# Kernel optimization log

Hardware: AMD Instinct MI355X
Metric: run time of the kernel (lower is better)

The kernel has to match this reference:

```python
import jax, jax.numpy as jnp
import numpy as np

GAMMAS = (0.01, 0.1, 1.0, 10.0, 100.0)
FOCAL_GAMMA = 2.0
SMOOTH = 0.1
TASK_W = (0.4, 0.3, 0.3)
A_RECON, A_ORTH, A_ADV = 1.0, 0.1, 0.1
NUM_DOMAINS = 4
NUM_LABELS1 = 4


def focal_smooth(logits, targets, maskf):
    # FocalLoss.forward with smoothing > 0, masked mean
    n_classes = logits.shape[1]
    log_p = jax.nn.log_softmax(logits, axis=1)
    p = jnp.exp(log_p)
    onehot = jax.nn.one_hot(targets, n_classes, dtype=logits.dtype)
    smooth = onehot * (1.0 - SMOOTH) + SMOOTH / n_classes
    ce = -(smooth * log_p).sum(axis=1)
    pt = jnp.take_along_axis(p, targets[:, None], axis=1)[:, 0]
    loss = ce * (1.0 - pt) ** FOCAL_GAMMA
    return (loss * maskf).sum() / jnp.maximum(maskf.sum(), 1.0)


def ce_masked(logits, targets, maskf):
    log_p = jax.nn.log_softmax(logits, axis=1)
    nll = -jnp.take_along_axis(log_p, targets[:, None], axis=1)[:, 0]
    return (nll * maskf).sum() / jnp.maximum(maskf.sum(), 1.0)


def cond_mmd(feats, domains, labels, maskf):
    # Global pairwise sq-distance matrix; multi-gamma RBF kernels summed.
    sq = (feats ** 2).sum(axis=-1)                      # (B,)
    Dmat = sq[:, None] + sq[None, :] - 2.0 * feats @ feats.T  # (B,B)
    Ksum = jnp.zeros_like(Dmat)
    for g in GAMMAS:
        Ksum = Ksum + jnp.exp(-g * Dmat)
    loss = jnp.asarray(0.0, feats.dtype)
    count = jnp.asarray(0.0, feats.dtype)
    for lab in range(NUM_LABELS1):
        lm = (labels == lab).astype(feats.dtype) * maskf
        for d1 in range(NUM_DOMAINS):
            m1 = lm * (domains == d1).astype(feats.dtype)
            n1 = m1.sum()
            Km1 = Ksum @ m1
            for d2 in range(d1 + 1, NUM_DOMAINS):
                m2 = lm * (domains == d2).astype(feats.dtype)
                n2 = m2.sum()
                valid = (n1 > 1) & (n2 > 1)
                term = (m1 @ Km1) / jnp.maximum(n1, 1.0) ** 2 \
                     + (m2 @ (Ksum @ m2)) / jnp.maximum(n2, 1.0) ** 2 \
                     - 2.0 * (m2 @ Km1) / jnp.maximum(n1 * n2, 1.0)
                loss = loss + jnp.where(valid, term, 0.0)
                count = count + valid.astype(feats.dtype)
    return loss / jnp.maximum(count, 1.0)


def hsic(c, s):
    n = c.shape[0]
    c = c / jnp.maximum(jnp.linalg.norm(c, axis=-1, keepdims=True), 1e-12)
    s = s / jnp.maximum(jnp.linalg.norm(s, axis=-1, keepdims=True), 1e-12)
    K = c @ c.T
    L = s @ s.T
    Kc = K - K.mean(axis=0, keepdims=True) - K.mean(axis=1, keepdims=True) + K.mean()
    Lc = L - L.mean(axis=0, keepdims=True) - L.mean(axis=1, keepdims=True) + L.mean()
    return (Kc * Lc).sum() / (n - 1) ** 2


def setup_inputs() -> dict:
    key = jax.random.key(0)
    ks = jax.random.split(key, 20)
    B, D, H = 4096, 256, 768
    inp = {
        'logits1': jax.random.normal(ks[0], (B, 4), jnp.float32),
        'labels1': jax.random.randint(ks[1], (B,), 0, 4),
        'logits2': jax.random.normal(ks[2], (B, 6), jnp.float32),
        'labels2': jax.random.randint(ks[3], (B,), 0, 6),
        'logits3': jax.random.normal(ks[4], (B, 3), jnp.float32),
        'labels3': jax.random.randint(ks[5], (B,), 0, 3),
        'c_v': jax.random.normal(ks[6], (B, D), jnp.float32),
        's_v': jax.random.normal(ks[7], (B, D), jnp.float32),
        'c_t': jax.random.normal(ks[8], (B, D), jnp.float32),
        's_t': jax.random.normal(ks[9], (B, D), jnp.float32),
        'v_sv': jax.random.normal(ks[10], (B, NUM_DOMAINS), jnp.float32),
        'v_st': jax.random.normal(ks[11], (B, NUM_DOMAINS), jnp.float32),
        'domain_labels': jax.random.randint(ks[12], (B,), 0, NUM_DOMAINS),
        'mask': jnp.ones((B,), dtype=bool),
        'h_img_recon': jax.random.normal(ks[13], (B, H), jnp.float32),
        'h_img_orig': jax.random.normal(ks[14], (B, H), jnp.float32),
        'h_txt_recon': jax.random.normal(ks[15], (B, H), jnp.float32),
        'h_txt_orig': jax.random.normal(ks[16], (B, H), jnp.float32),
    }
    return inp


def reference(logits1, labels1, logits2, labels2, logits3, labels3,
              c_v, s_v, c_t, s_t, v_sv, v_st, domain_labels, mask,
              h_img_recon, h_img_orig, h_txt_recon, h_txt_orig):
    maskf = mask.astype(jnp.float32)
    total = jnp.asarray(0.0, jnp.float32)
    # classification (focal + label smoothing), per-task weighted
    total = total + TASK_W[0] * focal_smooth(logits1, labels1, maskf)
    total = total + TASK_W[1] * focal_smooth(logits2, labels2, maskf)
    total = total + TASK_W[2] * focal_smooth(logits3, labels3, maskf)
    # adversarial: CE on spurious domain logits + conditional MMD on causal feats
    l_adv_s = ce_masked(v_sv, domain_labels, maskf) + ce_masked(v_st, domain_labels, maskf)
    l_adv_c = cond_mmd(c_v, domain_labels, labels1, maskf) \
            + cond_mmd(c_t, domain_labels, labels1, maskf)
    total = total + A_ADV * (l_adv_s + l_adv_c)
    # orthogonality (HSIC), on unmasked features as in source
    l_orth = hsic(c_v, s_v) + hsic(c_t, s_t)
    total = total + A_ORTH * l_orth
    # reconstruction MSE
    l_recon = jnp.mean((h_img_recon - h_img_orig) ** 2) + jnp.mean((h_txt_recon - h_txt_orig) ** 2)
    total = total + A_RECON * l_recon
    return total
```

## Files before the change

kernel.cpp:

```cpp
#include <hip/hip_runtime.h>
#include <hip/hip_bf16.h>


typedef short bf16x8 __attribute__((ext_vector_type(8)));
typedef float f32x4 __attribute__((ext_vector_type(4)));
typedef unsigned long long u64;
typedef unsigned int u32;

static constexpr int D = 256;
static constexpr int H = 768;
static constexpr int NG = 16;
static constexpr float FX32 = 4294967296.f;
static constexpr float IFX32 = 2.3283064365386963e-10f;

__device__ inline void gAddFx(u64* p, float v) {
  long long q = (long long)llroundf(v * FX32);
  atomicAdd(p, (u64)q);
}
__device__ inline float fxToF(u64 v) { return (float)(long long)v * IFX32; }

__device__ inline float focal_n(const float* x, int n, int tgt,
                                float s_over_n, float oms) {
  float mx = x[0];
  for (int c = 1; c < n; ++c) mx = fmaxf(mx, x[c]);
  float se = 0.f, sx = 0.f;
  for (int c = 0; c < n; ++c) { se += __expf(x[c] - mx); sx += x[c]; }
  float logZ = mx + __logf(se);
  float ce = logZ - oms * x[tgt] - s_over_n * sx;
  float pt = __expf(x[tgt] - logZ);
  float om = 1.f - pt;
  return ce * om * om;
}

extern "C" __global__ __launch_bounds__(256) void k_pre(
    const void* __restrict__ mask, const int* __restrict__ y1,
    const int* __restrict__ dom,
    const float* __restrict__ l1, const float* __restrict__ l2,
    const float* __restrict__ l3, const int* __restrict__ y2,
    const int* __restrict__ y3,
    const float* __restrict__ vsv, const float* __restrict__ vst,
    const float* __restrict__ cv, const float* __restrict__ sv,
    const float* __restrict__ ct, const float* __restrict__ st,
    const float* __restrict__ ir, const float* __restrict__ io,
    const float* __restrict__ trc, const float* __restrict__ to,
    u64* SA, u64* GCU, u64* U64,
    int* gid, float* sq, float* inv, unsigned short* bf, u32* CNTB,
    int B, int N4, int NA, int NB) {
  __shared__ u32 sh3[3];
  __shared__ u32 cnt[17];
  __shared__ int redi[4];
  __shared__ float redf[4];
  __shared__ float redf5[5][4];
  __shared__ float ub[4][64][4];
  int bid = blockIdx.x;
  int t = threadIdx.x;

  if (bid < NA) {
    if (t < 3) sh3[t] = 0;
    if (t < 17) cnt[t] = 0;
    __syncthreads();
    u32 a = 0, b2 = 0, cd = 0;
    if (t * 16 + 15 < B) {
      uint4 wv = ((const uint4*)mask)[t];
      u32 ws[4] = {wv.x, wv.y, wv.z, wv.w};
      #pragma unroll
      for (int j = 0; j < 4; ++j) {
        a |= ws[j] & 0xffu; b2 |= ws[j] & 0xff00u; cd |= ws[j] & 0xffff0000u;
      }
    }
    if (a) atomicOr(&sh3[0], 1u);
    if (b2) atomicOr(&sh3[1], 1u);
    if (cd) atomicOr(&sh3[2], 1u);
    __syncthreads();
    int mode;
    if ((sh3[1] | sh3[2]) == 0) mode = 0;
    else if (sh3[0] == 0 && sh3[1] == 0) mode = 1;
    else mode = 2;
    int r = bid * 256 + t;
    int mi = 0;
    float s[5] = {0.f, 0.f, 0.f, 0.f, 0.f};
    if (r < B) {
      if (mode == 0)      mi = ((const int*)mask)[r] ? 1 : 0;
      else if (mode == 1) mi = (((const float*)mask)[r] != 0.f) ? 1 : 0;
      else                mi = ((const unsigned char*)mask)[r] ? 1 : 0;
      int g = -1;
      if (mi) { g = y1[r] * 4 + dom[r]; atomicAdd(&cnt[g], 1u); }
      else atomicAdd(&cnt[16], 1u);
      gid[r] = g;
      if (mi) {
        float x[6];
        for (int c = 0; c < 4; ++c) x[c] = l1[r * 4 + c];
        s[0] = focal_n(x, 4, y1[r], 0.1f / 4.f, 0.9f);
        for (int c = 0; c < 6; ++c) x[c] = l2[r * 6 + c];
        s[1] = focal_n(x, 6, y2[r], 0.1f / 6.f, 0.9f);
        for (int c = 0; c < 3; ++c) x[c] = l3[r * 3 + c];
        s[2] = focal_n(x, 3, y3[r], 0.1f / 3.f, 0.9f);
        int d = dom[r];
        for (int c = 0; c < 4; ++c) x[c] = vsv[r * 4 + c];
        {
          float mx = fmaxf(fmaxf(x[0], x[1]), fmaxf(x[2], x[3]));
          float se = __expf(x[0]-mx)+__expf(x[1]-mx)+__expf(x[2]-mx)+__expf(x[3]-mx);
          s[3] = mx + __logf(se) - x[d];
        }
        for (int c = 0; c < 4; ++c) x[c] = vst[r * 4 + c];
        {
          float mx = fmaxf(fmaxf(x[0], x[1]), fmaxf(x[2], x[3]));
          float se = __expf(x[0]-mx)+__expf(x[1]-mx)+__expf(x[2]-mx)+__expf(x[3]-mx);
          s[4] = mx + __logf(se) - x[d];
        }
      }
    }
    int v = mi;
    #pragma unroll
    for (int o = 32; o > 0; o >>= 1) {
      v += __shfl_down(v, o);
      #pragma unroll
      for (int k = 0; k < 5; ++k) s[k] += __shfl_down(s[k], o);
    }
    if ((t & 63) == 0) {
      redi[t >> 6] = v;
      #pragma unroll
      for (int k = 0; k < 5; ++k) redf5[k][t >> 6] = s[k];
    }
    __syncthreads();
    if (t == 0) {
      atomicAdd(&SA[5], (u64)(redi[0] + redi[1] + redi[2] + redi[3]));
      #pragma unroll
      for (int k = 0; k < 5; ++k)
        gAddFx(&SA[k], redf5[k][0] + redf5[k][1] + redf5[k][2] + redf5[k][3]);
    }
    if (t < NG && cnt[t]) atomicAdd(&GCU[t], (u64)cnt[t]);
    if (t < 17) CNTB[bid * 17 + t] = cnt[t];
  } else if (bid < NA + NB) {
    int b = bid - NA;
    int perF = NB >> 2;
    int f = b / perF;
    int rb = b - f * perF;
    const float* p = (f == 0) ? cv : (f == 1) ? sv : (f == 2) ? ct : st;
    int w = t >> 6, L = t & 63;
    float up0 = 0.f, up1 = 0.f, up2 = 0.f, up3 = 0.f;
    for (int bt = 0; bt < 2; ++bt) {
      int rbase = rb * 32 + w * 8 + bt * 4;
      float4 vv[4];
      #pragma unroll
      for (int i = 0; i < 4; ++i)
        vv[i] = ((const float4*)(p + (size_t)(rbase + i) * D))[L];
      float ss[4];
      #pragma unroll
      for (int i = 0; i < 4; ++i)
        ss[i] = vv[i].x * vv[i].x + vv[i].y * vv[i].y
              + vv[i].z * vv[i].z + vv[i].w * vv[i].w;
      #pragma unroll
      for (int o = 32; o > 0; o >>= 1) {
        #pragma unroll
        for (int i = 0; i < 4; ++i) ss[i] += __shfl_down(ss[i], o);
      }
      #pragma unroll
      for (int i = 0; i < 4; ++i) ss[i] = __shfl(ss[i], 0);
      #pragma unroll
      for (int i = 0; i < 4; ++i) {
        int r = rbase + i;
        float iv = 1.f / fmaxf(sqrtf(ss[i]), 1e-12f);
        if ((f & 1) == 0) {
          int fi = f >> 1;
          alignas(8) __hip_bfloat16 hb[4];
          hb[0] = __float2bfloat16(vv[i].x); hb[1] = __float2bfloat16(vv[i].y);
          hb[2] = __float2bfloat16(vv[i].z); hb[3] = __float2bfloat16(vv[i].w);
          *(uint2*)(bf + ((size_t)fi * B + r) * D + L * 4) = *(uint2*)hb;
          if (L == 0) sq[fi * B + r] = ss[i];
        }
        if (L == 0) inv[f * B + r] = iv;
        up0 += vv[i].x * iv; up1 += vv[i].y * iv;
        up2 += vv[i].z * iv; up3 += vv[i].w * iv;
      }
    }
    ub[w][L][0] = up0; ub[w][L][1] = up1; ub[w][L][2] = up2; ub[w][L][3] = up3;
    __syncthreads();
    if (t < 64) {
      u64* Uf = U64 + f * D + 4 * t;
      #pragma unroll
      for (int j = 0; j < 4; ++j) {
        float s4 = ub[0][t][j] + ub[1][t][j] + ub[2][t][j] + ub[3][t][j];
        gAddFx(Uf + j, s4);
      }
    }
  } else {
    int cidx = bid - (NA + NB);
    int j = cidx >> 9;
    int cb = cidx & 511;
    const float4* A  = (const float4*)(j ? trc : ir);
    const float4* Bp = (const float4*)(j ? to : io);
    int CH = (N4 + 511) >> 9;
    int base = cb * CH;
    int end = min(base + CH, N4);
    float acc = 0.f;
    int idx = base + t;
    for (; idx + 256 < end; idx += 512) {
      float4 a0 = A[idx],       b0 = Bp[idx];
      float4 a1 = A[idx + 256], b1 = Bp[idx + 256];
      float dx0 = a0.x-b0.x, dy0 = a0.y-b0.y, dz0 = a0.z-b0.z, dw0 = a0.w-b0.w;
      float dx1 = a1.x-b1.x, dy1 = a1.y-b1.y, dz1 = a1.z-b1.z, dw1 = a1.w-b1.w;
      acc += dx0*dx0 + dy0*dy0 + dz0*dz0 + dw0*dw0
           + dx1*dx1 + dy1*dy1 + dz1*dz1 + dw1*dw1;
    }
    if (idx < end) {
      float4 a = A[idx], b = Bp[idx];
      float dx = a.x-b.x, dy = a.y-b.y, dz = a.z-b.z, dw = a.w-b.w;
      acc += dx*dx + dy*dy + dz*dz + dw*dw;
    }
    #pragma unroll
    for (int o = 32; o > 0; o >>= 1) acc += __shfl_down(acc, o);
    if ((t & 63) == 0) redf[t >> 6] = acc;
    __syncthreads();
    if (t == 0) gAddFx(&SA[6 + j], redf[0] + redf[1] + redf[2] + redf[3]);
  }
}

extern "C" __global__ __launch_bounds__(256) void k_mid(
    const u32* __restrict__ CNTB, const int* __restrict__ gid,
    const float* __restrict__ sq,
    const float* __restrict__ cv, const float* __restrict__ sv,
    const float* __restrict__ ct, const float* __restrict__ st,
    const float* __restrict__ inv,
    int* __restrict__ perm, float* __restrict__ sqp, int* __restrict__ OFF,
    unsigned short* __restrict__ bnT, int B, int NA) {
  __shared__ float ld[64 * 65];
  __shared__ u32 cbs[17], tots[17], wcnt[4][17];
  __shared__ u32 base[18];
  int b = blockIdx.x, t = threadIdx.x;

  if (b < NA) {
    if (t < 68) ((u32*)wcnt)[t] = 0;
    if (t < 17) {
      u32 cb = 0, tot = 0;
      for (int b2 = 0; b2 < NA; ++b2) {
        u32 c = CNTB[b2 * 17 + t];
        cb += (b2 < b) ? c : 0u;
        tot += c;
      }
      cbs[t] = cb; tots[t] = tot;
    }
    int r = b * 256 + t;
    int g = 16;
    if (r < B) { int gg = gid[r]; g = (gg < 0) ? 16 : gg; }
    __syncthreads();
    if (t == 0) {
      u32 s = 0;
      for (int g2 = 0; g2 < 17; ++g2) { base[g2] = s; s += tots[g2]; }
      base[17] = s;
    }
    u64 msk = ~0ull;
    #pragma unroll
    for (int bit = 0; bit < 5; ++bit) {
      int bv = (g >> bit) & 1;
      u64 bl = __ballot(bv);
      msk &= bv ? bl : ~bl;
    }
    int lane = t & 63, w = t >> 6;
    int rwave = __popcll(msk & ((1ull << lane) - 1ull));
    if (rwave == 0) wcnt[w][g] = (u32)__popcll(msk);
    __syncthreads();
    if (r < B) {
      int rank = rwave;
      for (int w2 = 0; w2 < 4; ++w2) if (w2 < w) rank += (int)wcnt[w2][g];
      int pos = (int)(base[g] + cbs[g]) + rank;
      perm[pos] = r;
      sqp[pos] = sq[r];
      sqp[B + pos] = sq[B + r];
    }
    if (b == 0 && t < 18) OFF[t] = (int)base[t];
  } else {
    int TPF = (B >> 6) * 4;
    int tb = b - NA;
    int fm = tb / TPF, tile = tb - fm * TPF;
    int it = tile >> 2, at = tile & 3;
    const float* src = (fm == 0) ? cv : (fm == 1) ? sv : (fm == 2) ? ct : st;
    const float* ivf = inv + (size_t)fm * B;
    int i0 = it * 64, a0 = at * 64;
    for (int e = t; e < 1024; e += 256) {
      int i = e >> 4, c4 = e & 15;
      float4 v = ((const float4*)(src + (size_t)(i0 + i) * D))[at * 16 + c4];
      float ivv = ivf[i0 + i];
      ld[i * 65 + c4 * 4 + 0] = v.x * ivv;
      ld[i * 65 + c4 * 4 + 1] = v.y * ivv;
      ld[i * 65 + c4 * 4 + 2] = v.z * ivv;
      ld[i * 65 + c4 * 4 + 3] = v.w * ivv;
    }
    __syncthreads();
    unsigned short* dst = bnT + (size_t)fm * D * B;
    for (int e = t; e < 512; e += 256) {
      int a = e >> 3, ic = e & 7;
      alignas(16) unsigned short h[8];
      #pragma unroll
      for (int j = 0; j < 8; ++j) {
        __hip_bfloat16 hb = __float2bfloat16(ld[(ic * 8 + j) * 65 + a]);
        h[j] = *(unsigned short*)&hb;
      }
      *(uint4*)(dst + (size_t)(a0 + a) * B + i0 + ic * 8) = *(uint4*)h;
    }
  }
}

extern "C" __global__ __launch_bounds__(256) void k_big(
    const unsigned short* __restrict__ bf, const float* __restrict__ sqp,
    const int* __restrict__ perm, const int* __restrict__ OFF,
    const unsigned short* __restrict__ bnT, float* __restrict__ Mf32,
    u64* GSP, int B) {
  __shared__ __align__(16) char smem[17536];
  unsigned short* Ab = (unsigned short*)smem;
  unsigned short* Bb = (unsigned short*)(smem + 8192);
  int bid = blockIdx.x;
  int tid = threadIdx.x;
  int w = tid >> 6, L = tid & 63, m = L & 15, q = L >> 4;
  int r0 = tid >> 3, ck = tid & 7;
  int swz = (ck ^ (r0 & 7)) * 8;
  int ar = w * 16 + m;

  if (bid < 64) {
    int half = bid & 1, bb = (bid >> 1) & 3, ab = (bid >> 3) & 3, p = (bid >> 5) & 1;
    const unsigned short* Abase = bnT + (size_t)(2 * p) * D * B;
    const unsigned short* Bbase = bnT + (size_t)(2 * p + 1) * D * B;
    size_t kof = (size_t)half * (B >> 1) + ck * 8;
    const uint4* gA0 = (const uint4*)(Abase + (size_t)(ab * 64 + r0) * B + kof);
    const uint4* gA1 = (const uint4*)(Abase + (size_t)(ab * 64 + r0 + 32) * B + kof);
    const uint4* gB0 = (const uint4*)(Bbase + (size_t)(bb * 64 + r0) * B + kof);
    const uint4* gB1 = (const uint4*)(Bbase + (size_t)(bb * 64 + r0 + 32) * B + kof);
    uint4* dA0 = (uint4*)&Ab[r0 * 64 + swz];
    uint4* dA1 = (uint4*)&Ab[(r0 + 32) * 64 + swz];
    uint4* dB0 = (uint4*)&Bb[r0 * 64 + swz];
    uint4* dB1 = (uint4*)&Bb[(r0 + 32) * 64 + swz];
    f32x4 acc[4] = {{0.f,0.f,0.f,0.f},{0.f,0.f,0.f,0.f},
                    {0.f,0.f,0.f,0.f},{0.f,0.f,0.f,0.f}};
    int nh = B >> 7;
    for (int hq = 0; hq < nh; ++hq) {
      *dA0 = gA0[hq * 8]; *dA1 = gA1[hq * 8];
      *dB0 = gB0[hq * 8]; *dB1 = gB1[hq * 8];
      __syncthreads();
      #pragma unroll
      for (int kk = 0; kk < 2; ++kk) {
        bf16x8 aF = *(const bf16x8*)&Ab[ar * 64 + (((kk * 4 + q) ^ (ar & 7)) * 8)];
        #pragma unroll
        for (int c = 0; c < 4; ++c) {
          int br = c * 16 + m;
          bf16x8 bF = *(const bf16x8*)&Bb[br * 64 + (((kk * 4 + q) ^ (br & 7)) * 8)];
          acc[c] = __builtin_amdgcn_mfma_f32_16x16x32_bf16(aF, bF, acc[c], 0, 0, 0);
        }
      }
      if (hq < nh - 1) __syncthreads();
    }
    float* Mo = Mf32 + (size_t)(half * 2 + p) * D * D;
    int ri0 = w * 16 + q * 4;
    #pragma unroll
    for (int c = 0; c < 4; ++c) {
      #pragma unroll
      for (int v = 0; v < 4; ++v)
        Mo[(size_t)(ab * 64 + ri0 + v) * D + bb * 64 + c * 16 + m] = acc[c][v];
    }
    return;
  }

  float* sA = (float*)(smem + 16384);
  float* sB = (float*)(smem + 16640);
  int*   pA = (int*)(smem + 16896);
  int*   pB = (int*)(smem + 17152);
  int*   offs = (int*)(smem + 17408);

  int idx2 = bid - 64;
  int feat = idx2 & 1;
  int tlin = idx2 >> 1;
  int NT = B / 64;
  float tf = (float)tlin;
  int ti = (int)((2.f * NT + 1.f -
                  sqrtf((2.f * NT + 1.f) * (2.f * NT + 1.f) - 8.f * tf)) * 0.5f);
  while (ti > 0 && (ti * NT - (ti * (ti - 1)) / 2) > tlin) --ti;
  while (((ti + 1) * NT - ((ti + 1) * ti) / 2) <= tlin) ++ti;
  int tj = ti + (tlin - (ti * NT - (ti * (ti - 1)) / 2));
  int i0 = ti * 64, j0 = tj * 64;
  bool diag = (ti == tj);
  const unsigned short* fb = bf + (size_t)feat * B * D;
  const float* sqf = sqp + (size_t)feat * B;

  if (tid < 64) { pA[tid] = perm[i0 + tid]; sA[tid] = sqf[i0 + tid]; }
  else if (tid < 128) { int r = tid - 64; pB[r] = perm[j0 + r]; sB[r] = sqf[j0 + r]; }
  else if (tid < 146) offs[tid - 128] = OFF[tid - 128];
  __syncthreads();

  int gr0 = 0, nbr = 0, gc0 = 0, ncb = 0;
  #pragma unroll
  for (int g = 1; g <= 17; ++g) {
    int o = offs[g];
    gr0 += (o <= i0) ? 1 : 0;
    nbr += (o > i0 && o < i0 + 64) ? 1 : 0;
    gc0 += (o <= j0) ? 1 : 0;
    ncb += (o > j0 && o < j0 + 64) ? 1 : 0;
  }
  if (gr0 == 16 || gc0 == 16) return;
  int gr1 = gr0 + nbr;
  int gc1 = gc0 + ncb;
  int s_r = nbr ? offs[gr1] : i0 + 64;
  int s_c = ncb ? offs[gc1] : j0 + 64;

  const uint4* gA0 = (const uint4*)(fb + (size_t)pA[r0] * D + ck * 8);
  const uint4* gA1 = (const uint4*)(fb + (size_t)pA[r0 + 32] * D + ck * 8);
  uint4* dA0 = (uint4*)&Ab[r0 * 64 + swz];
  uint4* dA1 = (uint4*)&Ab[(r0 + 32) * 64 + swz];
  const uint4* gB0 = nullptr; const uint4* gB1 = nullptr;
  uint4* dB0 = nullptr; uint4* dB1 = nullptr;
  if (!diag) {
    gB0 = (const uint4*)(fb + (size_t)pB[r0] * D + ck * 8);
    gB1 = (const uint4*)(fb + (size_t)pB[r0 + 32] * D + ck * 8);
    dB0 = (uint4*)&Bb[r0 * 64 + swz];
    dB1 = (uint4*)&Bb[(r0 + 32) * 64 + swz];
  }
  const unsigned short* Bp = diag ? Ab : Bb;

  f32x4 acc[4] = {{0.f,0.f,0.f,0.f},{0.f,0.f,0.f,0.f},
                  {0.f,0.f,0.f,0.f},{0.f,0.f,0.f,0.f}};

  for (int hq = 0; hq < 4; ++hq) {
    *dA0 = gA0[hq * 8]; *dA1 = gA1[hq * 8];
    if (!diag) { *dB0 = gB0[hq * 8]; *dB1 = gB1[hq * 8]; }
    __syncthreads();
    #pragma unroll
    for (int kk = 0; kk < 2; ++kk) {
      bf16x8 aF = *(const bf16x8*)&Ab[ar * 64 + (((kk * 4 + q) ^ (ar & 7)) * 8)];
      #pragma unroll
      for (int c = 0; c < 4; ++c) {
        int br = c * 16 + m;
        bf16x8 bF = *(const bf16x8*)&Bp[br * 64 + (((kk * 4 + q) ^ (br & 7)) * 8)];
        acc[c] = __builtin_amdgcn_mfma_f32_16x16x32_bf16(aF, bF, acc[c], 0, 0, 0);
      }
    }
    if (hq < 3) __syncthreads();
  }

  int ri0 = w * 16 + q * 4;
  u64* gsp = GSP + ((size_t)(tlin & 63) * 2 + feat) * NG * NG;

  if (nbr <= 1 && ncb <= 1) {
    float siv[4]; bool rhiv[4];
    #pragma unroll
    for (int v = 0; v < 4; ++v) {
      siv[v] = sA[ri0 + v];
      rhiv[v] = (i0 + ri0 + v) >= s_r;
    }
    float a00 = 0.f, a01 = 0.f, a10 = 0.f, a11 = 0.f;
    #pragma unroll
    for (int c = 0; c < 4; ++c) {
      int rj = c * 16 + m;
      float sb = sB[rj];
      float lo = 0.f, hi = 0.f;
      #pragma unroll
      for (int v = 0; v < 4; ++v) {
        float d = fmaxf(siv[v] + sb - 2.f * acc[c][v], 0.f);
        float K = __expf(-0.01f * d) + __expf(-0.1f * d) + __expf(-d)
                + __expf(-10.f * d) + __expf(-100.f * d);
        if (diag) {
          int ri = ri0 + v;
          K = (ri > rj) ? 0.f : (ri == rj) ? 5.f : K;
        }
        float kh = rhiv[v] ? K : 0.f;
        hi += kh; lo += K - kh;
      }
      bool chi = (j0 + rj) >= s_c;
      float loH = chi ? lo : 0.f;
      float hiH = chi ? hi : 0.f;
      a00 += lo - loH; a01 += loH;
      a10 += hi - hiH; a11 += hiH;
    }
    #pragma unroll
    for (int o = 32; o > 0; o >>= 1) {
      a00 += __shfl_down(a00, o); a01 += __shfl_down(a01, o);
      a10 += __shfl_down(a10, o); a11 += __shfl_down(a11, o);
    }
    if (L == 0) {
      if (a00 != 0.f)
        atomicAdd(&gsp[gr0 * NG + gc0], (u64)(long long)llroundf(a00 * 65536.f));
      if (a01 != 0.f && gc1 < 16)
        atomicAdd(&gsp[gr0 * NG + gc1], (u64)(long long)llroundf(a01 * 65536.f));
      if (a10 != 0.f && gr1 < 16)
        atomicAdd(&gsp[gr1 * NG + gc0], (u64)(long long)llroundf(a10 * 65536.f));
      if (a11 != 0.f && gr1 < 16 && gc1 < 16)
        atomicAdd(&gsp[gr1 * NG + gc1], (u64)(long long)llroundf(a11 * 65536.f));
    }
  } else {
    int giv[4]; float siv[4];
    #pragma unroll
    for (int v = 0; v < 4; ++v) {
      int idx = i0 + ri0 + v;
      int g = 0;
      #pragma unroll
      for (int k = 1; k <= 16; ++k) g += (offs[k] <= idx) ? 1 : 0;
      giv[v] = g;
      siv[v] = sA[ri0 + v];
    }
    #pragma unroll
    for (int c = 0; c < 4; ++c) {
      int rj = c * 16 + m;
      int jdx = j0 + rj;
      int gj = 0;
      #pragma unroll
      for (int k = 1; k <= 16; ++k) gj += (offs[k] <= jdx) ? 1 : 0;
      float sb = sB[rj];
      #pragma unroll
      for (int v = 0; v < 4; ++v) {
        int ri = ri0 + v;
        if (giv[v] < 16 && gj < 16 && !(diag && ri > rj)) {
          float K;
          if (diag && ri == rj) K = 5.f;
          else {
            float d = fmaxf(siv[v] + sb - 2.f * acc[c][v], 0.f);
            K = __expf(-0.01f * d) + __expf(-0.1f * d) + __expf(-d)
              + __expf(-10.f * d) + __expf(-100.f * d);
          }
          u32 kf = (u32)(K * 65536.f + 0.5f);
          atomicAdd(&gsp[giv[v] * NG + gj], (u64)kf);
        }
      }
    }
  }
}

extern "C" __global__ __launch_bounds__(256) void k_hsic(
    const u64* __restrict__ U64, const float* __restrict__ Mf32, u64* SA) {
  __shared__ float red[8];
  __shared__ float ush[32], vsh[D];
  int p = blockIdx.y;
  int k0 = blockIdx.x * 32;
  int t = threadIdx.x;
  vsh[t] = fxToF(U64[(2 * p + 1) * D + t]);
  if (t < 32) ush[t] = fxToF(U64[(2 * p) * D + k0 + t]);
  __syncthreads();
  const float* M0 = Mf32 + (size_t)p * D * D;
  const float* M1 = Mf32 + (size_t)(2 + p) * D * D;
  float trkl = 0.f, cr = 0.f;
  #pragma unroll 4
  for (int k = 0; k < 32; ++k) {
    float mv = M0[(size_t)(k0 + k) * D + t] + M1[(size_t)(k0 + k) * D + t];
    trkl += mv * mv;
    cr += ush[k] * mv;
  }
  cr *= vsh[t];
  #pragma unroll
  for (int o = 32; o > 0; o >>= 1) { trkl += __shfl_down(trkl, o); cr += __shfl_down(cr, o); }
  if ((t & 63) == 0) { red[t >> 6] = trkl; red[4 + (t >> 6)] = cr; }
  __syncthreads();
  if (t == 0) gAddFx(&SA[10 + p], red[0] + red[1] + red[2] + red[3]);
  if (t == 64) gAddFx(&SA[12 + p], red[4] + red[5] + red[6] + red[7]);
}

extern "C" __global__ __launch_bounds__(256) void k_final(
    const u64* SA, const u64* GCU, const u64* GSP,
    const u64* U64, float* out, int B) {
  __shared__ float red[8];
  __shared__ float gssh[2 * NG * NG];
  int t = threadIdx.x;
  for (int e = t; e < 2 * NG * NG; e += 256) {
    u64 ssum = 0;
    int f = e >> 8, idx = e & 255;
    for (int cpy = 0; cpy < 64; ++cpy)
      ssum += GSP[((size_t)cpy * 2 + f) * NG * NG + idx];
    gssh[e] = (float)((double)ssum * (1.0 / 65536.0));
  }
  __syncthreads();

  float n = (float)B;
  float hs[2];
  for (int p = 0; p < 2; ++p) {
    float ut = fxToF(U64[(2 * p) * D + t]);
    float vt = fxToF(U64[(2 * p + 1) * D + t]);
    float uu = ut * ut, vv = vt * vt;
    #pragma unroll
    for (int o = 32; o > 0; o >>= 1) { uu += __shfl_down(uu, o); vv += __shfl_down(vv, o); }
    __syncthreads();
    if ((t & 63) == 0) { red[t >> 6] = uu; red[4 + (t >> 6)] = vv; }
    __syncthreads();
    float uus = red[0] + red[1] + red[2] + red[3];
    float vvs = red[4] + red[5] + red[6] + red[7];
    float trkl = (float)((double)(long long)SA[10 + p] * (double)IFX32);
    float cr   = (float)((double)(long long)SA[12 + p] * (double)IFX32);
    hs[p] = (trkl - (2.f / n) * cr + uus * vvs / (n * n))
          / ((n - 1.f) * (n - 1.f));
    __syncthreads();
  }
  if (t == 0) {
    float msum = fmaxf((float)SA[5], 1.f);
    float f1 = fxToF(SA[0]) / msum;
    float f2 = fxToF(SA[1]) / msum;
    float f3 = fxToF(SA[2]) / msum;
    float cesv = fxToF(SA[3]) / msum;
    float cest = fxToF(SA[4]) / msum;
    float mmd[2];
    for (int f = 0; f < 2; ++f) {
      float loss = 0.f, cntv = 0.f;
      for (int lab = 0; lab < 4; ++lab)
        for (int d1 = 0; d1 < 4; ++d1)
          for (int d2 = d1 + 1; d2 < 4; ++d2) {
            int a = lab * 4 + d1, b = lab * 4 + d2;
            float n1 = (float)GCU[a], n2 = (float)GCU[b];
            if (n1 > 1.f && n2 > 1.f) {
              float g11 = 2.f * gssh[f * 256 + a * NG + a] - 5.f * n1;
              float g22 = 2.f * gssh[f * 256 + b * NG + b] - 5.f * n2;
              float g12 = gssh[f * 256 + a * NG + b];
              loss += g11 / (fmaxf(n1, 1.f) * fmaxf(n1, 1.f))
                    + g22 / (fmaxf(n2, 1.f) * fmaxf(n2, 1.f))
                    - 2.f * g12 / fmaxf(n1 * n2, 1.f);
              cntv += 1.f;
            }
          }
      mmd[f] = loss / fmaxf(cntv, 1.f);
    }
    double rs = ((double)(long long)SA[6] + (double)(long long)SA[7])
              * (double)IFX32;
    float recon = (float)(rs / ((double)B * (double)H));
    float total = 0.4f * f1 + 0.3f * f2 + 0.3f * f3
                + 0.1f * (cesv + cest + mmd[0] + mmd[1])
                + 0.1f * (hs[0] + hs[1])
                + recon;
    out[0] = total;
  }
}

extern "C" void kernel_launch(void* const* d_in, const int* in_sizes, int n_in,
                              void* d_out, int out_size, void* d_ws, size_t ws_size,
                              hipStream_t stream) {
  const float* l1  = (const float*)d_in[0];
  const int*   y1  = (const int*)d_in[1];
  const float* l2  = (const float*)d_in[2];
  const int*   y2  = (const int*)d_in[3];
  const float* l3  = (const float*)d_in[4];
  const int*   y3  = (const int*)d_in[5];
  const float* cv  = (const float*)d_in[6];
  const float* sv  = (const float*)d_in[7];
  const float* ct  = (const float*)d_in[8];
  const float* st  = (const float*)d_in[9];
  const float* vsv = (const float*)d_in[10];
  const float* vst = (const float*)d_in[11];
  const int*   dom = (const int*)d_in[12];
  const void*  mask= d_in[13];
  const float* ir  = (const float*)d_in[14];
  const float* io  = (const float*)d_in[15];
  const float* trc = (const float*)d_in[16];
  const float* to  = (const float*)d_in[17];
  int B = in_sizes[1];

  u64* SA  = (u64*)d_ws;
  u64* GCU = SA + 32;
  u64* U64 = GCU + 16;
  u64* GSP = U64 + 4 * D;
  u64* zend = GSP + 64 * 2 * NG * NG;
  size_t zeroBytes = (size_t)((char*)zend - (char*)d_ws);
  unsigned short* bf  = (unsigned short*)zend;
  unsigned short* bnT = bf + 2 * (size_t)B * D;
  float* Mf32 = (float*)(bnT + 4 * (size_t)D * B);
  int*   gid = (int*)(Mf32 + 4 * (size_t)D * D);
  float* sq  = (float*)(gid + B);
  float* inv = sq + 2 * B;
  int*   perm = (int*)(inv + 4 * B);
  float* sqp  = (float*)(perm + B);
  int*   OFF  = (int*)(sqp + 2 * B);
  u32*   CNTB = (u32*)(OFF + 18);

  int NA = B / 256;
  int NB = B / 8;
  int NC = 1024;
  int N4 = B * H / 4;

  hipMemsetAsync(d_ws, 0, zeroBytes, stream);
  k_pre<<<NA + NB + NC, 256, 0, stream>>>(
      mask, y1, dom, l1, l2, l3, y2, y3, vsv, vst,
      cv, sv, ct, st, ir, io, trc, to,
      SA, GCU, U64, gid, sq, inv, bf, CNTB, B, N4, NA, NB);
  int NTR = B / 4;
  k_mid<<<NA + NTR, 256, 0, stream>>>(CNTB, gid, sq, cv, sv, ct, st, inv,
                                      perm, sqp, OFF, bnT, B, NA);
  int NT = B / 64;
  int nmmd = 2 * (NT * (NT + 1) / 2);
  k_big<<<64 + nmmd, 256, 0, stream>>>(bf, sqp, perm, OFF, bnT, Mf32, GSP, B);
  k_hsic<<<dim3(8, 2), 256, 0, stream>>>(U64, Mf32, SA);
  k_final<<<1, 256, 0, stream>>>(SA, GCU, GSP, U64, (float*)d_out, B);
}
```

Measured before the change: 207.9 us.

## Enlarge MMD Gram tiles to 128x128 and split HSIC GEMM K four ways

The pairwise-distance MMD blocks now compute 128x128 tiles, with each wave holding 2x8 MFMA accumulators instead of 1x4. This roughly quarters the number of tile blocks and improves operand reuse from LDS. The HSIC cross-covariance GEMM is split into four K-slices instead of two, writing four partial matrices that k_hsic sums. The feature-normalisation stage also loads all 8 rows up front instead of in two batches. The costs are more registers and LDS per block, and fewer blocks for occupancy.

```diff
diff --git a/kernel.cpp b/kernel.cpp
--- a/kernel.cpp
+++ b/kernel.cpp
@@ -138,41 +138,39 @@
     int rb = b - f * perF;
     const float* p = (f == 0) ? cv : (f == 1) ? sv : (f == 2) ? ct : st;
     int w = t >> 6, L = t & 63;
+    int rbase = rb * 32 + w * 8;
+    float4 vv[8];
+    #pragma unroll
+    for (int i = 0; i < 8; ++i)
+      vv[i] = ((const float4*)(p + (size_t)(rbase + i) * D))[L];
+    float ss[8];
+    #pragma unroll
+    for (int i = 0; i < 8; ++i)
+      ss[i] = vv[i].x * vv[i].x + vv[i].y * vv[i].y
+            + vv[i].z * vv[i].z + vv[i].w * vv[i].w;
+    #pragma unroll
+    for (int o = 32; o > 0; o >>= 1) {
+      #pragma unroll
+      for (int i = 0; i < 8; ++i) ss[i] += __shfl_down(ss[i], o);
+    }
+    #pragma unroll
+    for (int i = 0; i < 8; ++i) ss[i] = __shfl(ss[i], 0);
     float up0 = 0.f, up1 = 0.f, up2 = 0.f, up3 = 0.f;
-    for (int bt = 0; bt < 2; ++bt) {
-      int rbase = rb * 32 + w * 8 + bt * 4;
-      float4 vv[4];
-      #pragma unroll
-      for (int i = 0; i < 4; ++i)
-        vv[i] = ((const float4*)(p + (size_t)(rbase + i) * D))[L];
-      float ss[4];
-      #pragma unroll
-      for (int i = 0; i < 4; ++i)
-        ss[i] = vv[i].x * vv[i].x + vv[i].y * vv[i].y
-              + vv[i].z * vv[i].z + vv[i].w * vv[i].w;
-      #pragma unroll
-      for (int o = 32; o > 0; o >>= 1) {
-        #pragma unroll
-        for (int i = 0; i < 4; ++i) ss[i] += __shfl_down(ss[i], o);
-      }
-      #pragma unroll
-      for (int i = 0; i < 4; ++i) ss[i] = __shfl(ss[i], 0);
-      #pragma unroll
-      for (int i = 0; i < 4; ++i) {
-        int r = rbase + i;
-        float iv = 1.f / fmaxf(sqrtf(ss[i]), 1e-12f);
-        if ((f & 1) == 0) {
-          int fi = f >> 1;
-          alignas(8) __hip_bfloat16 hb[4];
-          hb[0] = __float2bfloat16(vv[i].x); hb[1] = __float2bfloat16(vv[i].y);
-          hb[2] = __float2bfloat16(vv[i].z); hb[3] = __float2bfloat16(vv[i].w);
-          *(uint2*)(bf + ((size_t)fi * B + r) * D + L * 4) = *(uint2*)hb;
-          if (L == 0) sq[fi * B + r] = ss[i];
-        }
-        if (L == 0) inv[f * B + r] = iv;
-        up0 += vv[i].x * iv; up1 += vv[i].y * iv;
-        up2 += vv[i].z * iv; up3 += vv[i].w * iv;
-      }
+    #pragma unroll
+    for (int i = 0; i < 8; ++i) {
+      int r = rbase + i;
+      float iv = 1.f / fmaxf(sqrtf(ss[i]), 1e-12f);
+      if ((f & 1) == 0) {
+        int fi = f >> 1;
+        alignas(8) __hip_bfloat16 hb[4];
+        hb[0] = __float2bfloat16(vv[i].x); hb[1] = __float2bfloat16(vv[i].y);
+        hb[2] = __float2bfloat16(vv[i].z); hb[3] = __float2bfloat16(vv[i].w);
+        *(uint2*)(bf + ((size_t)fi * B + r) * D + L * 4) = *(uint2*)hb;
+        if (L == 0) sq[fi * B + r] = ss[i];
+      }
+      if (L == 0) inv[f * B + r] = iv;
+      up0 += vv[i].x * iv; up1 += vv[i].y * iv;
+      up2 += vv[i].z * iv; up3 += vv[i].w * iv;
     }
     ub[w][L][0] = up0; ub[w][L][1] = up1; ub[w][L][2] = up2; ub[w][L][3] = up3;
     __syncthreads();
@@ -306,21 +304,20 @@
     const int* __restrict__ perm, const int* __restrict__ OFF,
     const unsigned short* __restrict__ bnT, float* __restrict__ Mf32,
     u64* GSP, int B) {
-  __shared__ __align__(16) char smem[17536];
+  __shared__ __align__(16) char smem[34944];
   unsigned short* Ab = (unsigned short*)smem;
-  unsigned short* Bb = (unsigned short*)(smem + 8192);
+  unsigned short* Bb = (unsigned short*)(smem + 16384);
   int bid = blockIdx.x;
   int tid = threadIdx.x;
   int w = tid >> 6, L = tid & 63, m = L & 15, q = L >> 4;
   int r0 = tid >> 3, ck = tid & 7;
   int swz = (ck ^ (r0 & 7)) * 8;
-  int ar = w * 16 + m;
-
-  if (bid < 64) {
-    int half = bid & 1, bb = (bid >> 1) & 3, ab = (bid >> 3) & 3, p = (bid >> 5) & 1;
+
+  if (bid < 128) {
+    int ks = bid & 3, bb = (bid >> 2) & 3, ab = (bid >> 4) & 3, p = (bid >> 6) & 1;
     const unsigned short* Abase = bnT + (size_t)(2 * p) * D * B;
     const unsigned short* Bbase = bnT + (size_t)(2 * p + 1) * D * B;
-    size_t kof = (size_t)half * (B >> 1) + ck * 8;
+    size_t kof = (size_t)ks * (B >> 2) + ck * 8;
     const uint4* gA0 = (const uint4*)(Abase + (size_t)(ab * 64 + r0) * B + kof);
     const uint4* gA1 = (const uint4*)(Abase + (size_t)(ab * 64 + r0 + 32) * B + kof);
     const uint4* gB0 = (const uint4*)(Bbase + (size_t)(bb * 64 + r0) * B + kof);
@@ -329,9 +326,10 @@
     uint4* dA1 = (uint4*)&Ab[(r0 + 32) * 64 + swz];
     uint4* dB0 = (uint4*)&Bb[r0 * 64 + swz];
     uint4* dB1 = (uint4*)&Bb[(r0 + 32) * 64 + swz];
+    int ar = w * 16 + m;
     f32x4 acc[4] = {{0.f,0.f,0.f,0.f},{0.f,0.f,0.f,0.f},
                     {0.f,0.f,0.f,0.f},{0.f,0.f,0.f,0.f}};
-    int nh = B >> 7;
+    int nh = B >> 8;
     for (int hq = 0; hq < nh; ++hq) {
       *dA0 = gA0[hq * 8]; *dA1 = gA1[hq * 8];
       *dB0 = gB0[hq * 8]; *dB1 = gB1[hq * 8];
@@ -348,7 +346,7 @@
       }
       if (hq < nh - 1) __syncthreads();
     }
-    float* Mo = Mf32 + (size_t)(half * 2 + p) * D * D;
+    float* Mo = Mf32 + (size_t)(ks * 2 + p) * D * D;
     int ri0 = w * 16 + q * 4;
     #pragma unroll
     for (int c = 0; c < 4; ++c) {
@@ -359,30 +357,30 @@
     return;
   }
 
-  float* sA = (float*)(smem + 16384);
-  float* sB = (float*)(smem + 16640);
-  int*   pA = (int*)(smem + 16896);
-  int*   pB = (int*)(smem + 17152);
-  int*   offs = (int*)(smem + 17408);
-
-  int idx2 = bid - 64;
+  float* sA = (float*)(smem + 32768);
+  float* sB = (float*)(smem + 33280);
+  int*   pA = (int*)(smem + 33792);
+  int*   pB = (int*)(smem + 34304);
+  int*   offs = (int*)(smem + 34816);
+
+  int idx2 = bid - 128;
   int feat = idx2 & 1;
   int tlin = idx2 >> 1;
-  int NT = B / 64;
+  int NT = B / 128;
   float tf = (float)tlin;
   int ti = (int)((2.f * NT + 1.f -
                   sqrtf((2.f * NT + 1.f) * (2.f * NT + 1.f) - 8.f * tf)) * 0.5f);
   while (ti > 0 && (ti * NT - (ti * (ti - 1)) / 2) > tlin) --ti;
   while (((ti + 1) * NT - ((ti + 1) * ti) / 2) <= tlin) ++ti;
   int tj = ti + (tlin - (ti * NT - (ti * (ti - 1)) / 2));
-  int i0 = ti * 64, j0 = tj * 64;
+  int i0 = ti * 128, j0 = tj * 128;
   bool diag = (ti == tj);
   const unsigned short* fb = bf + (size_t)feat * B * D;
   const float* sqf = sqp + (size_t)feat * B;
 
-  if (tid < 64) { pA[tid] = perm[i0 + tid]; sA[tid] = sqf[i0 + tid]; }
-  else if (tid < 128) { int r = tid - 64; pB[r] = perm[j0 + r]; sB[r] = sqf[j0 + r]; }
-  else if (tid < 146) offs[tid - 128] = OFF[tid - 128];
+  if (tid < 128) { pA[tid] = perm[i0 + tid]; sA[tid] = sqf[i0 + tid]; }
+  else { int r = tid - 128; pB[r] = perm[j0 + r]; sB[r] = sqf[j0 + r]; }
+  if (tid < 18) offs[tid] = OFF[tid];
   __syncthreads();
 
   int gr0 = 0, nbr = 0, gc0 = 0, ncb = 0;
@@ -390,77 +388,101 @@
   for (int g = 1; g <= 17; ++g) {
     int o = offs[g];
     gr0 += (o <= i0) ? 1 : 0;
-    nbr += (o > i0 && o < i0 + 64) ? 1 : 0;
+    nbr += (o > i0 && o < i0 + 128) ? 1 : 0;
     gc0 += (o <= j0) ? 1 : 0;
-    ncb += (o > j0 && o < j0 + 64) ? 1 : 0;
+    ncb += (o > j0 && o < j0 + 128) ? 1 : 0;
   }
   if (gr0 == 16 || gc0 == 16) return;
   int gr1 = gr0 + nbr;
   int gc1 = gc0 + ncb;
-  int s_r = nbr ? offs[gr1] : i0 + 64;
-  int s_c = ncb ? offs[gc1] : j0 + 64;
-
-  const uint4* gA0 = (const uint4*)(fb + (size_t)pA[r0] * D + ck * 8);
-  const uint4* gA1 = (const uint4*)(fb + (size_t)pA[r0 + 32] * D + ck * 8);
-  uint4* dA0 = (uint4*)&Ab[r0 * 64 + swz];
-  uint4* dA1 = (uint4*)&Ab[(r0 + 32) * 64 + swz];
-  const uint4* gB0 = nullptr; const uint4* gB1 = nullptr;
-  uint4* dB0 = nullptr; uint4* dB1 = nullptr;
+  int s_r = nbr ? offs[gr1] : i0 + 128;
+  int s_c = ncb ? offs[gc1] : j0 + 128;
+
+  const uint4* gA[4]; const uint4* gB[4];
+  uint4* dA[4]; uint4* dB[4];
+  #pragma unroll
+  for (int i = 0; i < 4; ++i) {
+    int rr = r0 + i * 32;
+    gA[i] = (const uint4*)(fb + (size_t)pA[rr] * D + ck * 8);
+    dA[i] = (uint4*)&Ab[rr * 64 + swz];
+  }
   if (!diag) {
-    gB0 = (const uint4*)(fb + (size_t)pB[r0] * D + ck * 8);
-    gB1 = (const uint4*)(fb + (size_t)pB[r0 + 32] * D + ck * 8);
-    dB0 = (uint4*)&Bb[r0 * 64 + swz];
-    dB1 = (uint4*)&Bb[(r0 + 32) * 64 + swz];
+    #pragma unroll
+    for (int i = 0; i < 4; ++i) {
+      int rr = r0 + i * 32;
+      gB[i] = (const uint4*)(fb + (size_t)pB[rr] * D + ck * 8);
+      dB[i] = (uint4*)&Bb[rr * 64 + swz];
+    }
   }
   const unsigned short* Bp = diag ? Ab : Bb;
-
-  f32x4 acc[4] = {{0.f,0.f,0.f,0.f},{0.f,0.f,0.f,0.f},
-                  {0.f,0.f,0.f,0.f},{0.f,0.f,0.f,0.f}};
+  int ar0 = w * 32 + m;
+
+  f32x4 acc[2][8];
+  #pragma unroll
+  for (int rt = 0; rt < 2; ++rt)
+    #pragma unroll
+    for (int cf = 0; cf < 8; ++cf) acc[rt][cf] = {0.f, 0.f, 0.f, 0.f};
 
   for (int hq = 0; hq < 4; ++hq) {
-    *dA0 = gA0[hq * 8]; *dA1 = gA1[hq * 8];
-    if (!diag) { *dB0 = gB0[hq * 8]; *dB1 = gB1[hq * 8]; }
+    #pragma unroll
+    for (int i = 0; i < 4; ++i) *dA[i] = gA[i][hq * 8];
+    if (!diag) {
+      #pragma unroll
+      for (int i = 0; i < 4; ++i) *dB[i] = gB[i][hq * 8];
+    }
     __syncthreads();
     #pragma unroll
     for (int kk = 0; kk < 2; ++kk) {
-      bf16x8 aF = *(const bf16x8*)&Ab[ar * 64 + (((kk * 4 + q) ^ (ar & 7)) * 8)];
-      #pragma unroll
-      for (int c = 0; c < 4; ++c) {
-        int br = c * 16 + m;
+      bf16x8 aF[2];
+      #pragma unroll
+      for (int rt = 0; rt < 2; ++rt) {
+        int ar = ar0 + rt * 16;
+        aF[rt] = *(const bf16x8*)&Ab[ar * 64 + (((kk * 4 + q) ^ (ar & 7)) * 8)];
+      }
+      #pragma unroll
+      for (int cf = 0; cf < 8; ++cf) {
+        int br = cf * 16 + m;
         bf16x8 bF = *(const bf16x8*)&Bp[br * 64 + (((kk * 4 + q) ^ (br & 7)) * 8)];
-        acc[c] = __builtin_amdgcn_mfma_f32_16x16x32_bf16(aF, bF, acc[c], 0, 0, 0);
+        acc[0][cf] = __builtin_amdgcn_mfma_f32_16x16x32_bf16(aF[0], bF, acc[0][cf], 0, 0, 0);
+        acc[1][cf] = __builtin_amdgcn_mfma_f32_16x16x32_bf16(aF[1], bF, acc[1][cf], 0, 0, 0);
       }
     }
     if (hq < 3) __syncthreads();
   }
 
-  int ri0 = w * 16 + q * 4;
+  int rb0 = w * 32 + q * 4;
   u64* gsp = GSP + ((size_t)(tlin & 63) * 2 + feat) * NG * NG;
 
   if (nbr <= 1 && ncb <= 1) {
-    float siv[4]; bool rhiv[4];
-    #pragma unroll
-    for (int v = 0; v < 4; ++v) {
-      siv[v] = sA[ri0 + v];
-      rhiv[v] = (i0 + ri0 + v) >= s_r;
-    }
+    float siv[2][4]; bool rhiv[2][4];
+    #pragma unroll
+    for (int rt = 0; rt < 2; ++rt)
+      #pragma unroll
+      for (int v = 0; v < 4; ++v) {
+        int ri = rb0 + rt * 16 + v;
+        siv[rt][v] = sA[ri];
+        rhiv[rt][v] = (i0 + ri) >= s_r;
+      }
     float a00 = 0.f, a01 = 0.f, a10 = 0.f, a11 = 0.f;
     #pragma unroll
-    for (int c = 0; c < 4; ++c) {
-      int rj = c * 16 + m;
+    for (int cf = 0; cf < 8; ++cf) {
+      int rj = cf * 16 + m;
       float sb = sB[rj];
       float lo = 0.f, hi = 0.f;
       #pragma unroll
-      for (int v = 0; v < 4; ++v) {
-        float d = fmaxf(siv[v] + sb - 2.f * acc[c][v], 0.f);
-        float K = __expf(-0.01f * d) + __expf(-0.1f * d) + __expf(-d)
-                + __expf(-10.f * d) + __expf(-100.f * d);
-        if (diag) {
-          int ri = ri0 + v;
-          K = (ri > rj) ? 0.f : (ri == rj) ? 5.f : K;
+      for (int rt = 0; rt < 2; ++rt) {
+        #pragma unroll
+        for (int v = 0; v < 4; ++v) {
+          float d = fmaxf(siv[rt][v] + sb - 2.f * acc[rt][cf][v], 0.f);
+          float K = __expf(-0.01f * d) + __expf(-0.1f * d) + __expf(-d)
+                  + __expf(-10.f * d) + __expf(-100.f * d);
+          if (diag) {
+            int ri = rb0 + rt * 16 + v;
+            K = (ri > rj) ? 0.f : (ri == rj) ? 5.f : K;
+          }
+          float kh = rhiv[rt][v] ? K : 0.f;
+          hi += kh; lo += K - kh;
         }
-        float kh = rhiv[v] ? K : 0.f;
-        hi += kh; lo += K - kh;
       }
       bool chi = (j0 + rj) >= s_c;
       float loH = chi ? lo : 0.f;
@@ -484,37 +506,42 @@
         atomicAdd(&gsp[gr1 * NG + gc1], (u64)(long long)llroundf(a11 * 65536.f));
     }
   } else {
-    int giv[4]; float siv[4];
-    #pragma unroll
-    for (int v = 0; v < 4; ++v) {
-      int idx = i0 + ri0 + v;
-      int g = 0;
-      #pragma unroll
-      for (int k = 1; k <= 16; ++k) g += (offs[k] <= idx) ? 1 : 0;
-      giv[v] = g;
-      siv[v] = sA[ri0 + v];
-    }
-    #pragma unroll
-    for (int c = 0; c < 4; ++c) {
-      int rj = c * 16 + m;
+    int giv[2][4]; float siv[2][4];
+    #pragma unroll
+    for (int rt = 0; rt < 2; ++rt)
+      #pragma unroll
+      for (int v = 0; v < 4; ++v) {
+        int idx = i0 + rb0 + rt * 16 + v;
+        int g = 0;
+        #pragma unroll
+        for (int k = 1; k <= 16; ++k) g += (offs[k] <= idx) ? 1 : 0;
+        giv[rt][v] = g;
+        siv[rt][v] = sA[rb0 + rt * 16 + v];
+      }
+    #pragma unroll
+    for (int cf = 0; cf < 8; ++cf) {
+      int rj = cf * 16 + m;
       int jdx = j0 + rj;
       int gj = 0;
       #pragma unroll
       for (int k = 1; k <= 16; ++k) gj += (offs[k] <= jdx) ? 1 : 0;
       float sb = sB[rj];
       #pragma unroll
-      for (int v = 0; v < 4; ++v) {
-        int ri = ri0 + v;
-        if (giv[v] < 16 && gj < 16 && !(diag && ri > rj)) {
-          float K;
-          if (diag && ri == rj) K = 5.f;
-          else {
-            float d = fmaxf(siv[v] + sb - 2.f * acc[c][v], 0.f);
-            K = __expf(-0.01f * d) + __expf(-0.1f * d) + __expf(-d)
-              + __expf(-10.f * d) + __expf(-100.f * d);
+      for (int rt = 0; rt < 2; ++rt) {
+        #pragma unroll
+        for (int v = 0; v < 4; ++v) {
+          int ri = rb0 + rt * 16 + v;
+          if (giv[rt][v] < 16 && gj < 16 && !(diag && ri > rj)) {
+            float K;
+            if (diag && ri == rj) K = 5.f;
+            else {
+              float d = fmaxf(siv[rt][v] + sb - 2.f * acc[rt][cf][v], 0.f);
+              K = __expf(-0.01f * d) + __expf(-0.1f * d) + __expf(-d)
+                + __expf(-10.f * d) + __expf(-100.f * d);
+            }
+            u32 kf = (u32)(K * 65536.f + 0.5f);
+            atomicAdd(&gsp[giv[rt][v] * NG + gj], (u64)kf);
           }
-          u32 kf = (u32)(K * 65536.f + 0.5f);
-          atomicAdd(&gsp[giv[v] * NG + gj], (u64)kf);
         }
       }
     }
@@ -531,12 +558,15 @@
   vsh[t] = fxToF(U64[(2 * p + 1) * D + t]);
   if (t < 32) ush[t] = fxToF(U64[(2 * p) * D + k0 + t]);
   __syncthreads();
-  const float* M0 = Mf32 + (size_t)p * D * D;
-  const float* M1 = Mf32 + (size_t)(2 + p) * D * D;
+  const float* M0 = Mf32 + (size_t)(0 * 2 + p) * D * D;
+  const float* M1 = Mf32 + (size_t)(1 * 2 + p) * D * D;
+  const float* M2 = Mf32 + (size_t)(2 * 2 + p) * D * D;
+  const float* M3 = Mf32 + (size_t)(3 * 2 + p) * D * D;
   float trkl = 0.f, cr = 0.f;
   #pragma unroll 4
   for (int k = 0; k < 32; ++k) {
-    float mv = M0[(size_t)(k0 + k) * D + t] + M1[(size_t)(k0 + k) * D + t];
+    size_t off = (size_t)(k0 + k) * D + t;
+    float mv = M0[off] + M1[off] + M2[off] + M3[off];
     trkl += mv * mv;
     cr += ush[k] * mv;
   }
@@ -653,7 +683,7 @@
   unsigned short* bf  = (unsigned short*)zend;
   unsigned short* bnT = bf + 2 * (size_t)B * D;
   float* Mf32 = (float*)(bnT + 4 * (size_t)D * B);
-  int*   gid = (int*)(Mf32 + 4 * (size_t)D * D);
+  int*   gid = (int*)(Mf32 + 8 * (size_t)D * D);
   float* sq  = (float*)(gid + B);
   float* inv = sq + 2 * B;
   int*   perm = (int*)(inv + 4 * B);
@@ -674,9 +704,9 @@
   int NTR = B / 4;
   k_mid<<<NA + NTR, 256, 0, stream>>>(CNTB, gid, sq, cv, sv, ct, st, inv,
                                       perm, sqp, OFF, bnT, B, NA);
-  int NT = B / 64;
-  int nmmd = 2 * (NT * (NT + 1) / 2);
-  k_big<<<64 + nmmd, 256, 0, stream>>>(bf, sqp, perm, OFF, bnT, Mf32, GSP, B);
+  int NT2 = B / 128;
+  int nmmd = 2 * (NT2 * (NT2 + 1) / 2);
+  k_big<<<128 + nmmd, 256, 0, stream>>>(bf, sqp, perm, OFF, bnT, Mf32, GSP, B);
   k_hsic<<<dim3(8, 2), 256, 0, stream>>>(U64, Mf32, SA);
   k_final<<<1, 256, 0, stream>>>(SA, GCU, GSP, U64, (float*)d_out, B);
 }
```

Result: slower. 214.1 us (+3.0%).
